# Kernel optimization log

Hardware: AMD Instinct MI355X
Metric: run time of the kernel (lower is better)

## Reference

```python
import math
import jax, jax.numpy as jnp
import numpy as np

# ---- module constants (from init_kwargs / SpectralBias.__init__) ----
B, H, L, DH = 1, 16, 2048, 64
M_MODES, K_FREQ = 2, 6
HIDDEN, OUT = max(128, 2 * DH), 4 * M_MODES + 1  # 128, 9 (use_slope=True)
L_TRAIN, L_MAX = 2048, 1_000_000
W_MIN = 2.0 * math.pi / L_MAX
W_MAX = 2.0 * math.pi / L_TRAIN
OMEGAS = np.logspace(math.log10(W_MIN), math.log10(W_MAX), K_FREQ).astype(np.float32)
DELTA_STAR_MAX = float(L_TRAIN - 1)
WIDTH_MIN, WIDTH_MAX = 32.0, 256.0
C_SCALE, TAU, EPS = 0.01, 64.0, 1e-9


def setup_inputs() -> dict:
    key = jax.random.key(0)
    k0, k1, k2 = jax.random.split(key, 3)
    q = jax.random.normal(k0, (B, H, L, DH), jnp.float32)
    w1 = jax.random.normal(k1, (HIDDEN, DH), jnp.float32) * (DH ** -0.5)
    b1 = jnp.zeros((HIDDEN,), jnp.float32)
    w2 = jax.random.normal(k2, (OUT, HIDDEN), jnp.float32) * 0.02
    # _init_outputs: first M output biases initialized to linspace(-6, -4, M)
    b2 = jnp.zeros((OUT,), jnp.float32).at[:M_MODES].set(jnp.linspace(-6.0, -4.0, M_MODES))
    return {"q": q, "w1": w1, "b1": b1, "w2": w2, "b2": b2}


def reference(q, w1, b1, w2, b2):
    """Query-conditioned Fourier relative-position bias b[b,h,i,j] for Delta = i - j >= 0.

    Per-query MLP emits, for each of M modes: gate logit, soft center delta*,
    width sigma, amplitude c, plus one slope term. Bias is a Fourier bump
    sum_k a_k(sigma) * cos(omega_k * (Delta - delta*)) with its Delta-mean
    subtracted (subtract_b0), scaled by sigmoid(gate) * c_scale * softplus(c),
    plus an ALiBi-like slope -softplus(s) * Delta / tau. Zero for Delta < 0.
    """
    omegas = jnp.asarray(OMEGAS)                       # [K]
    # shared-across-heads MLP (Linear -> SiLU -> Linear)
    y = jax.nn.silu(q @ w1.T + b1) @ w2.T + b2         # [B,H,L,4M+1]
    p = jax.nn.sigmoid(y[..., :M_MODES])               # gates          [B,H,L,M]
    dstar = jax.nn.sigmoid(y[..., M_MODES:2 * M_MODES]) * DELTA_STAR_MAX
    sigma = WIDTH_MIN + jax.nn.sigmoid(y[..., 2 * M_MODES:3 * M_MODES]) * (WIDTH_MAX - WIDTH_MIN)
    c = C_SCALE * jax.nn.softplus(y[..., 3 * M_MODES:4 * M_MODES])
    slope = jax.nn.softplus(y[..., 4 * M_MODES])       # [B,H,L]

    # Gaussian spectral weights per mode: a_k = exp(-0.5 * omega_k^2 * sigma^2)
    a = jnp.exp(-0.5 * (omegas ** 2) * (sigma[..., None] ** 2))   # [B,H,L,M,K]
    a = a / (a.sum(-1, keepdims=True) + EPS)
    phase = omegas * dstar[..., None]                              # [B,H,L,M,K]
    amp = (p * c)[..., None] * a
    # collapse modes into per-query cos/sin coefficients
    coefC = (amp * jnp.cos(phase)).sum(-2)             # [B,H,L,K]
    coefS = (amp * jnp.sin(phase)).sum(-2)

    d_arr = jnp.arange(L, dtype=jnp.float32)
    # subtract_b0: mean of the bump over Delta in [0, L)
    cos_mean = jnp.cos(omegas[:, None] * d_arr).mean(-1)           # [K]
    sin_mean = jnp.sin(omegas[:, None] * d_arr).mean(-1)
    b0 = coefC @ cos_mean + coefS @ sin_mean           # [B,H,L]

    delta = d_arr[:, None] - d_arr[None, :]            # [L,L], i - j
    mask = delta >= 0.0
    dp = jnp.where(mask, delta, 0.0)
    cos_d = jnp.cos(omegas[:, None, None] * dp)        # [K,L,L]
    sin_d = jnp.sin(omegas[:, None, None] * dp)
    fourier = jnp.einsum('bhik,kij->bhij', coefC, cos_d) + jnp.einsum('bhik,kij->bhij', coefS, sin_d)
    bias = fourier - b0[..., None] - (slope[..., None] / TAU) * dp
    return jnp.where(mask, bias, 0.0)                  # [B,H,L,L]
```

## Files before the change

### kernel.cpp

```cpp
#include <hip/hip_runtime.h>
#include <math.h>


struct BiasParams {
    float omg[6];
    float omg2[6];
    float cw[6];
    float sw[6];
    float cmn[6];
    float smn[6];
};

__device__ __forceinline__ float sigmoidf_(float x) { return 1.0f / (1.0f + expf(-x)); }
__device__ __forceinline__ float softplusf_(float x) {
    return fmaxf(x, 0.0f) + log1pf(expf(-fabsf(x)));
}

__global__ __launch_bounds__(256) void sb_coef_kernel(
    const float* __restrict__ q,  const float* __restrict__ w1,
    const float* __restrict__ b1, const float* __restrict__ w2,
    const float* __restrict__ b2, float* __restrict__ ws, BiasParams P)
{
    __shared__ float pl[256 * 13];
    const int t    = threadIdx.x;
    const int lane = t & 63;
    const int w    = t >> 6;
    const int qid  = (blockIdx.x << 6) + lane;

    float qv[64];
    {
        const float4* qr = (const float4*)(q + ((size_t)qid << 6));
        #pragma unroll
        for (int j = 0; j < 16; ++j) {
            float4 v = qr[j];
            qv[4*j+0] = v.x; qv[4*j+1] = v.y; qv[4*j+2] = v.z; qv[4*j+3] = v.w;
        }
    }

    const int h0 = __builtin_amdgcn_readfirstlane(w << 5);
    const float* __restrict__ w1u = w1 + (size_t)h0 * 64;

    float part[9];
    #pragma unroll
    for (int o = 0; o < 9; ++o) part[o] = 0.f;

    #pragma unroll 4
    for (int h = 0; h < 32; ++h) {
        const float* __restrict__ wr = w1u + h * 64;
        float a0 = 0.f, a1 = 0.f, a2 = 0.f, a3 = 0.f;
        #pragma unroll
        for (int d = 0; d < 64; d += 4) {
            a0 = fmaf(qv[d+0], wr[d+0], a0);
            a1 = fmaf(qv[d+1], wr[d+1], a1);
            a2 = fmaf(qv[d+2], wr[d+2], a2);
            a3 = fmaf(qv[d+3], wr[d+3], a3);
        }
        float a = ((a0 + a1) + (a2 + a3)) + b1[h0 + h];
        a = a * sigmoidf_(a);
        #pragma unroll
        for (int o = 0; o < 9; ++o)
            part[o] = fmaf(a, w2[o * 128 + h0 + h], part[o]);
    }

    #pragma unroll
    for (int o = 0; o < 9; ++o) pl[t * 13 + o] = part[o];
    __syncthreads();

    if (w == 0) {
        float y[9];
        #pragma unroll
        for (int o = 0; o < 9; ++o)
            y[o] = b2[o] + pl[lane * 13 + o] + pl[(64 + lane) * 13 + o]
                 + pl[(128 + lane) * 13 + o] + pl[(192 + lane) * 13 + o];

        float C[6], S[6];
        #pragma unroll
        for (int k = 0; k < 6; ++k) { C[k] = 0.f; S[k] = 0.f; }
        float slope = softplusf_(y[8]);

        #pragma unroll
        for (int m = 0; m < 2; ++m) {
            float p   = sigmoidf_(y[m]);
            float dst = sigmoidf_(y[2 + m]) * 2047.0f;
            float sg  = 32.0f + sigmoidf_(y[4 + m]) * 224.0f;
            float cm  = 0.01f * softplusf_(y[6 + m]);
            float s2  = sg * sg;
            float a[6]; float asum = 0.f;
            #pragma unroll
            for (int k = 0; k < 6; ++k) { a[k] = expf(-0.5f * P.omg2[k] * s2); asum += a[k]; }
            float inv = 1.0f / (asum + 1e-9f);
            float pc  = p * cm;
            #pragma unroll
            for (int k = 0; k < 6; ++k) {
                float sn, cn;
                sincosf(P.omg[k] * dst, &sn, &cn);
                float amp = pc * (a[k] * inv);
                C[k] = fmaf(amp, cn, C[k]);
                S[k] = fmaf(amp, sn, S[k]);
            }
        }
        float b0 = 0.f;
        #pragma unroll
        for (int k = 0; k < 6; ++k) b0 += C[k] * P.cmn[k] + S[k] * P.smn[k];

        float* cf = ws + ((size_t)qid << 4);
        ((float4*)cf)[0] = make_float4(C[0], C[1], C[2], C[3]);
        ((float4*)cf)[1] = make_float4(C[4], C[5], S[0], S[1]);
        ((float4*)cf)[2] = make_float4(S[2], S[3], S[4], S[5]);
        ((float4*)cf)[3] = make_float4(b0, slope * (1.0f / 64.0f), 0.f, 0.f);
    }
}

__global__ __launch_bounds__(512) void sb_bias_kernel(
    const float* __restrict__ ws, float* __restrict__ out, BiasParams P)
{
    const int rid = blockIdx.x;
    const int i   = rid & 2047;
    const float* cf = ws + ((size_t)rid << 4);
    const float4 c0 = ((const float4*)cf)[0];
    const float4 c1 = ((const float4*)cf)[1];
    const float4 c2 = ((const float4*)cf)[2];
    const float4 c3 = ((const float4*)cf)[3];
    const float C[6] = {c0.x, c0.y, c0.z, c0.w, c1.x, c1.y};
    const float S[6] = {c1.z, c1.w, c2.x, c2.y, c2.z, c2.w};
    const float b0 = c3.x, slt = c3.y;

    const int j0 = threadIdx.x << 2;
    const int D0 = i - j0;
    float res[4];

    if (D0 < 0) {
        #pragma unroll
        for (int s = 0; s < 4; ++s) res[s] = 0.f;
    } else {
        float g[6], hh[6];
        #pragma unroll
        for (int k = 0; k < 6; ++k) {
            float sn, cn;
            __sincosf(P.omg[k] * (float)D0, &sn, &cn);
            g[k]  = fmaf(C[k], cn,  S[k] * sn);
            hh[k] = fmaf(S[k], cn, -C[k] * sn);
        }
        float e = fmaf(-slt, (float)D0, -b0);
        if (D0 >= 3) {
            #pragma unroll
            for (int s = 0; s < 4; ++s) {
                res[s] = (((g[0] + g[1]) + (g[2] + g[3])) + (g[4] + g[5])) + e;
                if (s < 3) {
                    e += slt;
                    #pragma unroll
                    for (int k = 0; k < 6; ++k) {
                        float gn = fmaf(g[k],  P.cw[k], -hh[k] * P.sw[k]);
                        float hn = fmaf(hh[k], P.cw[k],  g[k]  * P.sw[k]);
                        g[k] = gn; hh[k] = hn;
                    }
                }
            }
        } else {
            #pragma unroll
            for (int s = 0; s < 4; ++s) {
                float four = ((g[0] + g[1]) + (g[2] + g[3])) + (g[4] + g[5]);
                res[s] = (s <= D0) ? (four + e) : 0.f;
                if (s < 3) {
                    e += slt;
                    #pragma unroll
                    for (int k = 0; k < 6; ++k) {
                        float gn = fmaf(g[k],  P.cw[k], -hh[k] * P.sw[k]);
                        float hn = fmaf(hh[k], P.cw[k],  g[k]  * P.sw[k]);
                        g[k] = gn; hh[k] = hn;
                    }
                }
            }
        }
    }
    float4* op = (float4*)(out + (((size_t)rid) << 11) + j0);
    op[0] = make_float4(res[0], res[1], res[2], res[3]);
}

extern "C" void kernel_launch(void* const* d_in, const int* in_sizes, int n_in,
                              void* d_out, int out_size, void* d_ws, size_t ws_size,
                              hipStream_t stream) {
    const float* q  = (const float*)d_in[0];
    const float* w1 = (const float*)d_in[1];
    const float* b1 = (const float*)d_in[2];
    const float* w2 = (const float*)d_in[3];
    const float* b2 = (const float*)d_in[4];
    float* out = (float*)d_out;
    float* ws  = (float*)d_ws;

    BiasParams P;
    const double l0 = log10(2.0 * M_PI / 1.0e6);
    const double l1 = log10(2.0 * M_PI / 2048.0);
    for (int k = 0; k < 6; ++k) {
        double e  = l0 + (l1 - l0) * ((double)k / 5.0);
        float  wf = (float)pow(10.0, e);
        P.omg[k]  = wf;
        P.omg2[k] = wf * wf;
        P.cw[k]   = (float)cos((double)wf);
        P.sw[k]   = (float)sin((double)wf);
        double cm = 0.0, sm = 0.0;
        for (int d = 0; d < 2048; ++d) { cm += cos((double)wf * d); sm += sin((double)wf * d); }
        P.cmn[k] = (float)(cm / 2048.0);
        P.smn[k] = (float)(sm / 2048.0);
    }

    sb_coef_kernel<<<512, 256, 0, stream>>>(q, w1, b1, w2, b2, ws, P);
    sb_bias_kernel<<<16 * 2048, 512, 0, stream>>>(ws, out, P);
}
```

Before: 311.4 us.

## Separate cos(w(i-j)) into per-row and per-column terms, tile bias kernel over row chunks

Uses the angle-difference identity to fold the query position i into per-row coefficients G/H in the coefficient kernel. The bias kernel then precomputes per-column sin/cos once per thread and reuses them across 32 rows, so each output is just 12 FMAs with no per-element sincos or rotation recurrence. Blocks that lie entirely above the diagonal write zeros without computing. The trade-offs are more registers per thread (48 cached trig values), fewer and larger blocks, and possible precision loss from large-argument products like w*i in float.

```diff
diff --git a/kernel.cpp b/kernel.cpp
--- a/kernel.cpp
+++ b/kernel.cpp
@@ -5,8 +5,6 @@
 struct BiasParams {
     float omg[6];
     float omg2[6];
-    float cw[6];
-    float sw[6];
     float cmn[6];
     float smn[6];
 };
@@ -103,78 +101,105 @@
         #pragma unroll
         for (int k = 0; k < 6; ++k) b0 += C[k] * P.cmn[k] + S[k] * P.smn[k];
 
+        const float fi = (float)(qid & 2047);
+        float G[6], Hh[6];
+        #pragma unroll
+        for (int k = 0; k < 6; ++k) {
+            float si, ci;
+            sincosf(P.omg[k] * fi, &si, &ci);
+            G[k]  = fmaf(C[k], ci,  S[k] * si);
+            Hh[k] = fmaf(C[k], si, -S[k] * ci);
+        }
+        const float slt = slope * (1.0f / 64.0f);
+        const float cst = fmaf(-slt, fi, -b0);
+
         float* cf = ws + ((size_t)qid << 4);
-        ((float4*)cf)[0] = make_float4(C[0], C[1], C[2], C[3]);
-        ((float4*)cf)[1] = make_float4(C[4], C[5], S[0], S[1]);
-        ((float4*)cf)[2] = make_float4(S[2], S[3], S[4], S[5]);
-        ((float4*)cf)[3] = make_float4(b0, slope * (1.0f / 64.0f), 0.f, 0.f);
-    }
-}
-
-__global__ __launch_bounds__(512) void sb_bias_kernel(
+        ((float4*)cf)[0] = make_float4(G[0], G[1], G[2], G[3]);
+        ((float4*)cf)[1] = make_float4(G[4], G[5], Hh[0], Hh[1]);
+        ((float4*)cf)[2] = make_float4(Hh[2], Hh[3], Hh[4], Hh[5]);
+        ((float4*)cf)[3] = make_float4(slt, cst, 0.f, 0.f);
+    }
+}
+
+__global__ __launch_bounds__(256) void sb_bias_kernel(
     const float* __restrict__ ws, float* __restrict__ out, BiasParams P)
 {
-    const int rid = blockIdx.x;
-    const int i   = rid & 2047;
-    const float* cf = ws + ((size_t)rid << 4);
-    const float4 c0 = ((const float4*)cf)[0];
-    const float4 c1 = ((const float4*)cf)[1];
-    const float4 c2 = ((const float4*)cf)[2];
-    const float4 c3 = ((const float4*)cf)[3];
-    const float C[6] = {c0.x, c0.y, c0.z, c0.w, c1.x, c1.y};
-    const float S[6] = {c1.z, c1.w, c2.x, c2.y, c2.z, c2.w};
-    const float b0 = c3.x, slt = c3.y;
-
-    const int j0 = threadIdx.x << 2;
-    const int D0 = i - j0;
-    float res[4];
-
-    if (D0 < 0) {
-        #pragma unroll
-        for (int s = 0; s < 4; ++s) res[s] = 0.f;
+    const int bid   = blockIdx.x;
+    const int strip = bid & 1;
+    const int chunk = (bid >> 1) & 63;
+    const int h     = bid >> 7;
+    const int j0s   = strip << 10;
+    const int i0    = chunk << 5;
+    const int jt    = j0s + (threadIdx.x << 2);
+
+    float4* op = (float4*)(out + (((size_t)((h << 11) + i0)) << 11) + jt);
+    const ptrdiff_t rowstep = 512;
+
+    if (i0 + 31 < j0s) {
+        const float4 z = make_float4(0.f, 0.f, 0.f, 0.f);
+        #pragma unroll 8
+        for (int r = 0; r < 32; ++r) { *op = z; op += rowstep; }
+        return;
+    }
+
+    float cb[4][6], sb[4][6];
+    #pragma unroll
+    for (int s = 0; s < 4; ++s) {
+        const float fj = (float)(jt + s);
+        #pragma unroll
+        for (int k = 0; k < 6; ++k) sincosf(P.omg[k] * fj, &sb[s][k], &cb[s][k]);
+    }
+    const float fj0 = (float)jt;
+    const float* cf = ws + (((size_t)((h << 11) + i0)) << 4);
+
+    if (i0 >= j0s + 1023) {
+        for (int r = 0; r < 32; ++r) {
+            const float4 a0 = ((const float4*)cf)[0];
+            const float4 a1 = ((const float4*)cf)[1];
+            const float4 a2 = ((const float4*)cf)[2];
+            const float4 a3 = ((const float4*)cf)[3];
+            const float G[6] = {a0.x, a0.y, a0.z, a0.w, a1.x, a1.y};
+            const float H[6] = {a1.z, a1.w, a2.x, a2.y, a2.z, a2.w};
+            const float slt = a3.x, cst = a3.y;
+            float res[4];
+            #pragma unroll
+            for (int s = 0; s < 4; ++s) {
+                float acc = fmaf(slt, fj0 + (float)s, cst);
+                #pragma unroll
+                for (int k = 0; k < 6; ++k) {
+                    acc = fmaf(G[k], cb[s][k], acc);
+                    acc = fmaf(H[k], sb[s][k], acc);
+                }
+                res[s] = acc;
+            }
+            *op = make_float4(res[0], res[1], res[2], res[3]);
+            op += rowstep; cf += 16;
+        }
     } else {
-        float g[6], hh[6];
-        #pragma unroll
-        for (int k = 0; k < 6; ++k) {
-            float sn, cn;
-            __sincosf(P.omg[k] * (float)D0, &sn, &cn);
-            g[k]  = fmaf(C[k], cn,  S[k] * sn);
-            hh[k] = fmaf(S[k], cn, -C[k] * sn);
-        }
-        float e = fmaf(-slt, (float)D0, -b0);
-        if (D0 >= 3) {
+        for (int r = 0; r < 32; ++r) {
+            const float4 a0 = ((const float4*)cf)[0];
+            const float4 a1 = ((const float4*)cf)[1];
+            const float4 a2 = ((const float4*)cf)[2];
+            const float4 a3 = ((const float4*)cf)[3];
+            const float G[6] = {a0.x, a0.y, a0.z, a0.w, a1.x, a1.y};
+            const float H[6] = {a1.z, a1.w, a2.x, a2.y, a2.z, a2.w};
+            const float slt = a3.x, cst = a3.y;
+            const int di = (i0 + r) - jt;
+            float res[4];
             #pragma unroll
             for (int s = 0; s < 4; ++s) {
-                res[s] = (((g[0] + g[1]) + (g[2] + g[3])) + (g[4] + g[5])) + e;
-                if (s < 3) {
-                    e += slt;
-                    #pragma unroll
-                    for (int k = 0; k < 6; ++k) {
-                        float gn = fmaf(g[k],  P.cw[k], -hh[k] * P.sw[k]);
-                        float hn = fmaf(hh[k], P.cw[k],  g[k]  * P.sw[k]);
-                        g[k] = gn; hh[k] = hn;
-                    }
+                float acc = fmaf(slt, fj0 + (float)s, cst);
+                #pragma unroll
+                for (int k = 0; k < 6; ++k) {
+                    acc = fmaf(G[k], cb[s][k], acc);
+                    acc = fmaf(H[k], sb[s][k], acc);
                 }
+                res[s] = (s <= di) ? acc : 0.f;
             }
-        } else {
-            #pragma unroll
-            for (int s = 0; s < 4; ++s) {
-                float four = ((g[0] + g[1]) + (g[2] + g[3])) + (g[4] + g[5]);
-                res[s] = (s <= D0) ? (four + e) : 0.f;
-                if (s < 3) {
-                    e += slt;
-                    #pragma unroll
-                    for (int k = 0; k < 6; ++k) {
-                        float gn = fmaf(g[k],  P.cw[k], -hh[k] * P.sw[k]);
-                        float hn = fmaf(hh[k], P.cw[k],  g[k]  * P.sw[k]);
-                        g[k] = gn; hh[k] = hn;
-                    }
-                }
-            }
-        }
-    }
-    float4* op = (float4*)(out + (((size_t)rid) << 11) + j0);
-    op[0] = make_float4(res[0], res[1], res[2], res[3]);
+            *op = make_float4(res[0], res[1], res[2], res[3]);
+            op += rowstep; cf += 16;
+        }
+    }
 }
 
 extern "C" void kernel_launch(void* const* d_in, const int* in_sizes, int n_in,
@@ -196,8 +221,6 @@
         float  wf = (float)pow(10.0, e);
         P.omg[k]  = wf;
         P.omg2[k] = wf * wf;
-        P.cw[k]   = (float)cos((double)wf);
-        P.sw[k]   = (float)sin((double)wf);
         double cm = 0.0, sm = 0.0;
         for (int d = 0; d < 2048; ++d) { cm += cos((double)wf * d); sm += sin((double)wf * d); }
         P.cmn[k] = (float)(cm / 2048.0);
@@ -205,5 +228,5 @@
     }
 
     sb_coef_kernel<<<512, 256, 0, stream>>>(q, w1, b1, w2, b2, ws, P);
-    sb_bias_kernel<<<16 * 2048, 512, 0, stream>>>(ws, out, P);
-}
+    sb_bias_kernel<<<2048, 256, 0, stream>>>(ws, out, P);
+}
```

New measurement: 315.2 us. Within noise of the previous version (+1.2%).
